# Kernel tuning notes

Measured on AMD Instinct MI355X. Metric: run time of the kernel, lower is better.

Reference implementation:

```python
import jax, jax.numpy as jnp
import numpy as np

B, T = 256, 64
L, S = 1024, 512          # large / small LSTM cell sizes
NC = 239                  # num classes
EPS = 1e-5                # BatchNorm eps (inference mode, mean=0, var=1)
TAU = 1.0                 # gumbel-softmax temperature


def setup_inputs() -> dict:
    key = jax.random.key(0)
    ks = jax.random.split(key, 12)
    def N(i, shape, s=0.05):
        return jax.random.normal(ks[i], shape, dtype=jnp.float32) * s
    return {
        "x": N(0, (B, T, 2048), 1.0),
        "x_small": N(1, (B, T, 1280), 1.0),
        # proj_mlp: Linear(2048->2048) + BN(2048) [inference] + ReLU
        "W_p": N(2, (2048, 2048)), "b_p": jnp.zeros(2048),
        "g_p": jnp.ones(2048), "be_p": jnp.zeros(2048),
        # small_proj_mlp: Linear(1280->512) + BN(512) + ReLU
        "W_s": N(3, (512, 1280)), "b_s": jnp.zeros(512),
        "g_s": jnp.ones(512), "be_s": jnp.zeros(512),
        # large LSTMCell: input 2048+512 -> hidden L
        "Wih_l": N(4, (4 * L, 2048 + 512)), "Whh_l": N(5, (4 * L, L)),
        "bih_l": jnp.zeros(4 * L), "bhh_l": jnp.zeros(4 * L),
        # small LSTMCell: input 512 -> hidden S
        "Wih_s": N(6, (4 * S, 512)), "Whh_s": N(7, (4 * S, S)),
        "bih_s": jnp.zeros(4 * S), "bhh_s": jnp.zeros(4 * S),
        # gate linear: (512 + 2L) -> 2
        "W_g": N(8, (2, 512 + 2 * L)), "b_g": jnp.zeros(2),
        # classifier: L -> NC
        "W_c": N(9, (NC, L)), "b_c": jnp.zeros(NC),
    }


def _bn_relu(x, gamma, beta):
    # inference BatchNorm1d with running_mean=0, running_var=1
    return jax.nn.relu(x * (gamma / np.sqrt(1.0 + EPS)) + beta)


def _lstm_cell(xin, h, c, Wih, Whh, bih, bhh):
    gates = xin @ Wih.T + bih + h @ Whh.T + bhh
    i, f, g, o = jnp.split(gates, 4, axis=1)
    c2 = jax.nn.sigmoid(f) * c + jax.nn.sigmoid(i) * jnp.tanh(g)
    h2 = jax.nn.sigmoid(o) * jnp.tanh(c2)
    return h2, c2


def reference(x, x_small, W_p, b_p, g_p, be_p, W_s, b_s, g_s, be_s,
              Wih_l, Whh_l, bih_l, bhh_l, Wih_s, Whh_s, bih_s, bhh_s,
              W_g, b_g, W_c, b_c):
    # project all frames at once (time-parallel part of the net)
    feats = _bn_relu(jnp.einsum('bti,oi->bto', x, W_p) + b_p, g_p, be_p)        # [B,T,2048]
    sfeats = _bn_relu(jnp.einsum('bti,oi->bto', x_small, W_s) + b_s, g_s, be_s)  # [B,T,512]

    def step(carry, ft_st):
        h_l, c_l, h_s, c_s = carry
        f_t, s_t = ft_st                                   # [B,2048], [B,512]
        h_s2, c_s2 = _lstm_cell(s_t, h_s, c_s, Wih_s, Whh_s, bih_s, bhh_s)
        # gating on OLD large state
        p = jax.nn.log_softmax(jnp.concatenate([s_t, h_l, c_l], 1) @ W_g.T + b_g, axis=1)
        y_soft = jax.nn.softmax(p / TAU, axis=1)
        y_hard = jax.nn.one_hot(jnp.argmax(y_soft, axis=1), 2, dtype=y_soft.dtype)
        r = y_hard + y_soft - jax.lax.stop_gradient(y_soft)  # straight-through hard sample
        h_ln, c_ln = _lstm_cell(jnp.concatenate([f_t, s_t], 1), h_l, c_l,
                                Wih_l, Whh_l, bih_l, bhh_l)
        ph = jnp.concatenate([h_s2[:, :S], h_l[:, S:L]], 1)  # partial (skip) hidden
        pc = jnp.concatenate([c_s2[:, :S], c_l[:, S:L]], 1)
        h_l2 = r[:, 0:1] * h_ln + r[:, 1:2] * ph
        c_l2 = r[:, 0:1] * c_ln + r[:, 1:2] * pc
        return (h_l2, c_l2, h_s2, c_s2), r

    z_l = jnp.zeros((B, L), jnp.float32)
    z_s = jnp.zeros((B, S), jnp.float32)
    (h_l, c_l, _, _), r_stack = jax.lax.scan(
        step, (z_l, z_l, z_s, z_s),
        (feats.transpose(1, 0, 2), sfeats.transpose(1, 0, 2)))
    logits = h_l @ W_c.T + b_c                             # [B,NC]
    return logits, r_stack                                 # r_stack: [T,B,2]
```

## Files before the change

kernel.cpp:

```cpp
#include <hip/hip_runtime.h>
#include <math.h>


typedef _Float16 f16;
typedef _Float16 f16x4 __attribute__((ext_vector_type(4)));
typedef _Float16 f16x8 __attribute__((ext_vector_type(8)));
typedef float f32x4 __attribute__((ext_vector_type(4)));

__device__ __forceinline__ float sigf(float x) { return 1.0f / (1.0f + expf(-x)); }

__device__ __forceinline__ void gload16(const f16* g, f16* l) {
  __builtin_amdgcn_global_load_lds((const __attribute__((address_space(1))) void*)g,
                                   (__attribute__((address_space(3))) void*)l, 16, 0, 0);
}

__global__ __launch_bounds__(256) void pack_img(const float* __restrict__ src,
    int C, int KT, int t0, int map, f16* __restrict__ dh, f16* __restrict__ dl,
    int slots)
{
  int gid = blockIdx.x * 256 + threadIdx.x;
  if (gid >= slots) return;
  int lane = gid & 63;
  int j = (gid >> 6) & 7;
  int pk = gid >> 9;
  int p = pk / KT, kt = pk - p * KT;
  int r = p * 128 + j * 16 + (lane & 15);
  int rg = map ? (((r & 255) << 6) + t0 + (r >> 8)) : r;
  int c = kt * 32 + (lane >> 4) * 8;
  const float* s = src + (long long)rg * C + c;
  float4 v0 = *(const float4*)s, v1 = *(const float4*)(s + 4);
  f16x8 h, l;
  h[0]=(f16)v0.x; l[0]=(f16)(v0.x-(float)h[0]);
  h[1]=(f16)v0.y; l[1]=(f16)(v0.y-(float)h[1]);
  h[2]=(f16)v0.z; l[2]=(f16)(v0.z-(float)h[2]);
  h[3]=(f16)v0.w; l[3]=(f16)(v0.w-(float)h[3]);
  h[4]=(f16)v1.x; l[4]=(f16)(v1.x-(float)h[4]);
  h[5]=(f16)v1.y; l[5]=(f16)(v1.y-(float)h[5]);
  h[6]=(f16)v1.z; l[6]=(f16)(v1.z-(float)h[6]);
  h[7]=(f16)v1.w; l[7]=(f16)(v1.w-(float)h[7]);
  *(f16x8*)(dh + (long long)gid * 8) = h;
  *(f16x8*)(dl + (long long)gid * 8) = l;
}

template <int BN, int EPI>
__device__ __forceinline__ void gcore(
    int pA, int pB,
    const f16* __restrict__ Ah0, const f16* __restrict__ Al0, int KT0,
    const f16* __restrict__ Ah1, const f16* __restrict__ Al1, int KT1,
    const f16* __restrict__ Bh, const f16* __restrict__ Bl, int KTB,
    float* __restrict__ C, int ldc, const float* __restrict__ G,
    f16* __restrict__ Ch, f16* __restrict__ Cl, int KTout,
    const float* __restrict__ e0, const float* __restrict__ e1,
    const float* __restrict__ e2)
{
  constexpr int WAVES = BN / 32;
  constexpr int WN = BN / 64;
  constexpr int NBU = BN / 16;
  constexpr int U = 16 + BN / 8;
  constexpr int NU = U / WAVES;
  __shared__ __align__(16) f16 smem[2][U * 512];

  const int tid = threadIdx.x;
  const int w = tid >> 6, lane = tid & 63;
  const int wr = w / WN, wc = w % WN;
  const int fr = lane & 15, fq = lane >> 4;
  const int nt = KT0 + KT1;

  const f16* up[NU];
  auto setptrs = [&](int kt) {
#pragma unroll
    for (int i = 0; i < NU; ++i) {
      const int u = w * NU + i;
      const f16* src;
      if (u < 16) {
        const int j = u & 7;
        const f16* AH = Ah0; const f16* AL = Al0; int KT = KT0, ktl = kt;
        if (KT1 > 0 && kt >= KT0) { AH = Ah1; AL = Al1; KT = KT1; ktl = kt - KT0; }
        src = ((u < 8) ? AH : AL) + (((long long)pA * KT + ktl) * 8 + j) * 512;
      } else {
        const int j = u - 16;
        const f16* IMG = (j < NBU) ? Bh : Bl;
        const int jb = (j < NBU) ? j : j - NBU;
        const int panel = pB * (BN / 128) + (jb >> 3);
        src = IMG + (((long long)panel * KTB + kt) * 8 + (jb & 7)) * 512;
      }
      up[i] = src + lane * 8;
    }
  };
  auto stage = [&](int buf) {
#pragma unroll
    for (int i = 0; i < NU; ++i) {
      gload16(up[i], &smem[buf][(w * NU + i) * 512]);
      up[i] += 4096;
    }
  };

  f32x4 acc[4][4];
#pragma unroll
  for (int m = 0; m < 4; ++m)
#pragma unroll
    for (int n = 0; n < 4; ++n) acc[m][n] = (f32x4){0.f, 0.f, 0.f, 0.f};

  setptrs(0);
  stage(0);
  __syncthreads();
  int cur = 0;
  for (int kt = 0; kt < nt; ++kt) {
    if (kt + 1 < nt) {
      if (KT1 > 0 && kt + 1 == KT0) setptrs(kt + 1);
      stage(cur ^ 1);
    }
    const f16* sb = smem[cur];
    f16x8 bh_[4], bl_[4];
#pragma unroll
    for (int n = 0; n < 4; ++n) {
      const int jb = wc * 4 + n;
      bh_[n] = *(const f16x8*)&sb[(16 + jb) * 512 + lane * 8];
      bl_[n] = *(const f16x8*)&sb[(16 + NBU + jb) * 512 + lane * 8];
    }
#pragma unroll
    for (int m = 0; m < 4; ++m) {
      const int ja = wr * 4 + m;
      f16x8 ah = *(const f16x8*)&sb[ja * 512 + lane * 8];
      f16x8 al = *(const f16x8*)&sb[(8 + ja) * 512 + lane * 8];
#pragma unroll
      for (int n = 0; n < 4; ++n) {
        acc[m][n] = __builtin_amdgcn_mfma_f32_16x16x32_f16(ah, bh_[n], acc[m][n], 0, 0, 0);
        acc[m][n] = __builtin_amdgcn_mfma_f32_16x16x32_f16(ah, bl_[n], acc[m][n], 0, 0, 0);
        acc[m][n] = __builtin_amdgcn_mfma_f32_16x16x32_f16(al, bh_[n], acc[m][n], 0, 0, 0);
      }
    }
    __syncthreads();
    cur ^= 1;
  }

  if constexpr (EPI == 1 || EPI == 2) {
#pragma unroll
    for (int m = 0; m < 4; ++m) {
#pragma unroll
      for (int n = 0; n < 4; ++n) {
        const int col = pB * BN + wc * 64 + n * 16 + fr;
        const float add = (EPI == 1) ? (e0[col] + e1[col]) : 0.f;
#pragma unroll
        for (int r = 0; r < 4; ++r) {
          const int row = pA * 128 + wr * 64 + m * 16 + fq * 4 + r;
          const long long idx = (long long)row * ldc + col;
          float v = acc[m][n][r] + add;
          if (EPI == 2) v += G[idx];
          C[idx] = v;
        }
      }
    }
  } else {
    float* cb = (float*)smem;
    const int CBLD = 132;
    for (int h = 0; h < 2; ++h) {
      if (wr == h) {
#pragma unroll
        for (int m = 0; m < 4; ++m) {
#pragma unroll
          for (int n = 0; n < 4; ++n) {
            const int colL = wc * 64 + n * 16 + fr;
            const int colG = pB * 128 + colL;
            const float p0 = e0[colG], p1 = e1[colG] * 0.99999500003750f,
                        p2 = e2[colG];
#pragma unroll
            for (int r = 0; r < 4; ++r) {
              const int rq = m * 16 + fq * 4 + r;
              cb[rq * CBLD + colL] = fmaxf((acc[m][n][r] + p0) * p1 + p2, 0.f);
            }
          }
        }
      }
      __syncthreads();
#pragma unroll
      for (int jl = 0; jl < 4; ++jl) {
        const float* s = &cb[(jl * 16 + fr) * CBLD + w * 32 + fq * 8];
        float4 v0 = *(const float4*)s, v1 = *(const float4*)(s + 4);
        float vv[8] = {v0.x, v0.y, v0.z, v0.w, v1.x, v1.y, v1.z, v1.w};
        f16x8 hh, ll;
#pragma unroll
        for (int e = 0; e < 8; ++e) {
          hh[e] = (f16)vv[e]; ll[e] = (f16)(vv[e] - (float)hh[e]);
        }
        const long long o =
            (((long long)pA * KTout + pB * 4 + w) * 8 + (h * 4 + jl)) * 512
            + lane * 8;
        *(f16x8*)(Ch + o) = hh;
        *(f16x8*)(Cl + o) = ll;
      }
      __syncthreads();
    }
  }
}

template <int BN, int EPI>
__global__ __launch_bounds__(BN * 2) void gmm_k(
    int gB, int swz,
    const f16* __restrict__ Ah0, const f16* __restrict__ Al0, int KT0,
    const f16* __restrict__ Ah1, const f16* __restrict__ Al1, int KT1,
    const f16* __restrict__ Bh, const f16* __restrict__ Bl, int KTB,
    float* __restrict__ C, int ldc, const float* __restrict__ G,
    f16* __restrict__ Ch, f16* __restrict__ Cl, int KTout,
    const float* __restrict__ e0, const float* __restrict__ e1,
    const float* __restrict__ e2)
{
  const int lin = blockIdx.x;
  int pA, pB;
  if (swz) {
    const int xc = lin & 7, j = lin >> 3, cpx = gB >> 3;
    pB = xc * cpx + (j % cpx);
    pA = j / cpx;
  } else {
    pB = lin % gB;
    pA = lin / gB;
  }
  gcore<BN, EPI>(pA, pB, Ah0, Al0, KT0, Ah1, Al1, KT1, Bh, Bl, KTB,
                 C, ldc, G, Ch, Cl, KTout, e0, e1, e2);
}

__global__ __launch_bounds__(256) void stepg_k(
    const f16* __restrict__ hlh, const f16* __restrict__ hll,
    const f16* __restrict__ hsh, const f16* __restrict__ hsl,
    const f16* __restrict__ Whlh, const f16* __restrict__ Whll,
    const f16* __restrict__ Whsh, const f16* __restrict__ Whsl,
    const float* __restrict__ Gl, const float* __restrict__ Gs,
    float* __restrict__ gl, float* __restrict__ gs)
{
  const int lin = blockIdx.x;
  const int xc = lin & 7, j = lin >> 3;
  const f16 *Ah, *Al, *Bh, *Bl;
  const float* G; float* C;
  int KT, ldc, pA, pB;
  if (j < 8) {
    pA = j >> 2; pB = xc * 4 + (j & 3);
    Ah = hlh; Al = hll; Bh = Whlh; Bl = Whll; KT = 32; ldc = 4096;
    C = gl; G = Gl;
  } else {
    const int jj = j - 8;
    pA = jj >> 1; pB = xc * 2 + (jj & 1);
    Ah = hsh; Al = hsl; Bh = Whsh; Bl = Whsl; KT = 16; ldc = 2048;
    C = gs; G = Gs;
  }
  gcore<128, 2>(pA, pB, Ah, Al, KT, nullptr, nullptr, 0, Bh, Bl, KT,
                C, ldc, G, nullptr, nullptr, 0, nullptr, nullptr, nullptr);
}

__global__ __launch_bounds__(256) void zs_img_k(const f16* __restrict__ sfh,
    const f16* __restrict__ sfl, const float* __restrict__ Wg,
    float* __restrict__ zs, int t0)
{
  const int wv = threadIdx.x >> 6, lane = threadIdx.x & 63;
  const int rr = blockIdx.x * 4 + wv;
  const int p = rr >> 7, j = (rr >> 4) & 7, fr = rr & 15;
  const int kt = lane >> 2, fq = lane & 3;
  const long long a = (((long long)p * 16 + kt) * 8 + j) * 512 + (fq * 16 + fr) * 8;
  f16x8 h8 = *(const f16x8*)(sfh + a);
  f16x8 l8 = *(const f16x8*)(sfl + a);
  const int k0 = kt * 32 + fq * 8;
  float z0 = 0.f, z1 = 0.f;
#pragma unroll
  for (int i = 0; i < 8; ++i) {
    float s = (float)h8[i] + (float)l8[i];
    z0 += s * Wg[k0 + i]; z1 += s * Wg[2560 + k0 + i];
  }
#pragma unroll
  for (int off = 32; off > 0; off >>= 1) {
    z0 += __shfl_down(z0, off);
    z1 += __shfl_down(z1, off);
  }
  if (lane == 0) {
    const int bt = ((rr & 255) << 6) + t0 + (rr >> 8);
    zs[bt * 2] = z0; zs[bt * 2 + 1] = z1;
  }
}

__global__ __launch_bounds__(256) void step_upd(
    const float* __restrict__ gl, const float* __restrict__ gs,
    const float* __restrict__ hl_o, const float* __restrict__ cl_o,
    const float* __restrict__ cs_o,
    float* __restrict__ hl_n, float* __restrict__ cl_n,
    float* __restrict__ hs_n, float* __restrict__ cs_n,
    f16* __restrict__ hlIh, f16* __restrict__ hlIl,
    f16* __restrict__ hsIh, f16* __restrict__ hsIl,
    const float* __restrict__ zs, const float* __restrict__ Wg,
    const float* __restrict__ bg, float* __restrict__ rout, int t)
{
  const int b = blockIdx.x, tid = threadIdx.x;
  __shared__ float red0[256], red1[256];
  __shared__ float shs[512], scs[512];
  __shared__ float rsh[2];

  const int pb = b >> 7, jb = (b >> 4) & 7, frb = b & 15;

  float4 h4 = *(const float4*)(hl_o + (long long)b * 1024 + tid * 4);
  float4 c4 = *(const float4*)(cl_o + (long long)b * 1024 + tid * 4);
  float4 w0h = *(const float4*)(Wg + 512 + tid * 4);
  float4 w0c = *(const float4*)(Wg + 1536 + tid * 4);
  float4 w1h = *(const float4*)(Wg + 2560 + 512 + tid * 4);
  float4 w1c = *(const float4*)(Wg + 2560 + 1536 + tid * 4);
  red0[tid] = h4.x * w0h.x + h4.y * w0h.y + h4.z * w0h.z + h4.w * w0h.w
            + c4.x * w0c.x + c4.y * w0c.y + c4.z * w0c.z + c4.w * w0c.w;
  red1[tid] = h4.x * w1h.x + h4.y * w1h.y + h4.z * w1h.z + h4.w * w1h.w
            + c4.x * w1c.x + c4.y * w1c.y + c4.z * w1c.z + c4.w * w1c.w;

  {
    const float* gb = gs + (long long)b * 2048;
#pragma unroll
    for (int e = 0; e < 2; ++e) {
      const int n = tid * 2 + e;
      float gi = gb[n], gf = gb[512 + n], gg = gb[1024 + n], go = gb[1536 + n];
      float c2 = sigf(gf) * cs_o[b * 512 + n] + sigf(gi) * tanhf(gg);
      float h2 = sigf(go) * tanhf(c2);
      shs[n] = h2; scs[n] = c2;
      hs_n[b * 512 + n] = h2; cs_n[b * 512 + n] = c2;
      const int kt = n >> 5, fqn = (n >> 3) & 3, en = n & 7;
      const long long o = (((long long)pb * 16 + kt) * 8 + jb) * 512
                        + (fqn * 16 + frb) * 8 + en;
      f16 hh = (f16)h2;
      hsIh[o] = hh; hsIl[o] = (f16)(h2 - (float)hh);
    }
  }
  __syncthreads();
  for (int s = 128; s > 0; s >>= 1) {
    if (tid < s) { red0[tid] += red0[tid + s]; red1[tid] += red1[tid + s]; }
    __syncthreads();
  }
  if (tid == 0) {
    float z0 = red0[0] + zs[(b * 64 + t) * 2 + 0] + bg[0];
    float z1 = red1[0] + zs[(b * 64 + t) * 2 + 1] + bg[1];
    int hard = (z1 > z0) ? 1 : 0;
    rsh[0] = hard ? 0.0f : 1.0f; rsh[1] = hard ? 1.0f : 0.0f;
    rout[b * 2 + 0] = rsh[0]; rout[b * 2 + 1] = rsh[1];
  }
  __syncthreads();
  const float r0 = rsh[0], r1 = rsh[1];

  {
    const float* glb = gl + (long long)b * 4096;
    const int n = tid * 4;
    float4 gi4 = *(const float4*)(glb + n);
    float4 gf4 = *(const float4*)(glb + 1024 + n);
    float4 gg4 = *(const float4*)(glb + 2048 + n);
    float4 go4 = *(const float4*)(glb + 3072 + n);
    float4 co4 = *(const float4*)(cl_o + (long long)b * 1024 + n);
    float4 ho4 = *(const float4*)(hl_o + (long long)b * 1024 + n);
    float gi[4] = {gi4.x, gi4.y, gi4.z, gi4.w};
    float gf[4] = {gf4.x, gf4.y, gf4.z, gf4.w};
    float gg[4] = {gg4.x, gg4.y, gg4.z, gg4.w};
    float go[4] = {go4.x, go4.y, go4.z, go4.w};
    float co[4] = {co4.x, co4.y, co4.z, co4.w};
    float ho[4] = {ho4.x, ho4.y, ho4.z, ho4.w};
    float hv[4], cv[4];
    f16x4 ih, il;
#pragma unroll
    for (int e = 0; e < 4; ++e) {
      float cln = sigf(gf[e]) * co[e] + sigf(gi[e]) * tanhf(gg[e]);
      float hln = sigf(go[e]) * tanhf(cln);
      float ph = (n + e < 512) ? shs[n + e] : ho[e];
      float pc = (n + e < 512) ? scs[n + e] : co[e];
      hv[e] = r0 * hln + r1 * ph;
      cv[e] = r0 * cln + r1 * pc;
      ih[e] = (f16)hv[e]; il[e] = (f16)(hv[e] - (float)ih[e]);
    }
    float4 hw = {hv[0], hv[1], hv[2], hv[3]};
    float4 cw = {cv[0], cv[1], cv[2], cv[3]};
    *(float4*)(hl_n + (long long)b * 1024 + n) = hw;
    *(float4*)(cl_n + (long long)b * 1024 + n) = cw;
    const int kt = n >> 5, fqn = (n >> 3) & 3, en = n & 7;
    const long long o = (((long long)pb * 32 + kt) * 8 + jb) * 512
                      + (fqn * 16 + frb) * 8 + en;
    *(f16x4*)(hlIh + o) = ih;
    *(f16x4*)(hlIl + o) = il;
  }
}

__global__ __launch_bounds__(256) void logits_k(const float* __restrict__ hl,
                                                const float* __restrict__ Wc,
                                                const float* __restrict__ bc,
                                                float* __restrict__ out)
{
  __shared__ float hsd[1024];
  const int b = blockIdx.x, tid = threadIdx.x;
  *(float4*)(hsd + tid * 4) = *(const float4*)(hl + (long long)b * 1024 + tid * 4);
  __syncthreads();
  if (tid < 239) {
    const float* w = Wc + (long long)tid * 1024;
    float s = 0.0f;
    for (int k = 0; k < 1024; k += 4) {
      float4 wv = *(const float4*)(w + k);
      s += hsd[k] * wv.x + hsd[k + 1] * wv.y + hsd[k + 2] * wv.z + hsd[k + 3] * wv.w;
    }
    out[(long long)b * 239 + tid] = s + bc[tid];
  }
}

#define BKK 32
template <int BM, int BN, int TM, int TN, int EPI>
__global__ __launch_bounds__(256) void gemm_nt(
    int M, int N,
    const float* __restrict__ A0, long long as0, const float* __restrict__ B0, long long bs0, int K0,
    const float* __restrict__ A1, long long as1, const float* __restrict__ B1, long long bs1, int K1,
    const float* __restrict__ A2, long long as2, const float* __restrict__ B2, long long bs2, int K2,
    float* __restrict__ C, long long ldc,
    const float* __restrict__ e0, const float* __restrict__ e1, const float* __restrict__ e2)
{
  __shared__ float As[BKK][BM + 4];
  __shared__ float Bs[BKK][BN + 4];
  const int tid = threadIdx.x;
  const int m0 = blockIdx.x * BM;
  const int n0 = blockIdx.y * BN;
  constexpr int C4 = BKK / 4;
  constexpr int RPP = 256 / C4;
  constexpr int APASS = BM / RPP;
  constexpr int BPASS = BN / RPP;
  const int lr = tid / C4;
  const int lc = tid % C4;
  float4 pa[APASS], pb[BPASS];
  const int nt = (K0 + K1 + K2) / BKK;
  auto load = [&](int kt) {
    const int kg = kt * BKK;
    const float* ap; long long as_; const float* bp; long long bs_;
    if (kg < K0)           { ap = A0 + kg;          as_ = as0; bp = B0 + kg;          bs_ = bs0; }
    else if (kg < K0 + K1) { int kl = kg - K0;      ap = A1 + kl; as_ = as1; bp = B1 + kl; bs_ = bs1; }
    else                   { int kl = kg - K0 - K1; ap = A2 + kl; as_ = as2; bp = B2 + kl; bs_ = bs2; }
#pragma unroll
    for (int p = 0; p < APASS; p++) {
      int r = lr + p * RPP;
      pa[p] = *(const float4*)(ap + (long long)(m0 + r) * as_ + lc * 4);
    }
#pragma unroll
    for (int p = 0; p < BPASS; p++) {
      int r = lr + p * RPP;
      pb[p] = *(const float4*)(bp + (long long)(n0 + r) * bs_ + lc * 4);
    }
  };
  const int tx = tid % (BN / TN);
  const int ty = tid / (BN / TN);
  float acc[TM][TN];
#pragma unroll
  for (int i = 0; i < TM; i++)
#pragma unroll
    for (int j = 0; j < TN; j++) acc[i][j] = 0.0f;
  load(0);
  for (int kt = 0; kt < nt; ++kt) {
    __syncthreads();
#pragma unroll
    for (int p = 0; p < APASS; p++) {
      int r = lr + p * RPP;
      As[lc * 4 + 0][r] = pa[p].x; As[lc * 4 + 1][r] = pa[p].y;
      As[lc * 4 + 2][r] = pa[p].z; As[lc * 4 + 3][r] = pa[p].w;
    }
#pragma unroll
    for (int p = 0; p < BPASS; p++) {
      int r = lr + p * RPP;
      Bs[lc * 4 + 0][r] = pb[p].x; Bs[lc * 4 + 1][r] = pb[p].y;
      Bs[lc * 4 + 2][r] = pb[p].z; Bs[lc * 4 + 3][r] = pb[p].w;
    }
    __syncthreads();
    if (kt + 1 < nt) load(kt + 1);
#pragma unroll
    for (int k = 0; k < BKK; k++) {
      float a[TM], bfr[TN];
#pragma unroll
      for (int i = 0; i < TM; i++) a[i] = As[k][ty * TM + i];
#pragma unroll
      for (int j = 0; j < TN; j++) bfr[j] = Bs[k][tx * TN + j];
#pragma unroll
      for (int i = 0; i < TM; i++)
#pragma unroll
        for (int j = 0; j < TN; j++) acc[i][j] += a[i] * bfr[j];
    }
  }
#pragma unroll
  for (int i = 0; i < TM; i++) {
    const int m = m0 + ty * TM + i;
    const int n = n0 + tx * TN;
    float v[TN];
#pragma unroll
    for (int j = 0; j < TN; j++) {
      float a = acc[i][j];
      if (EPI == 0) {
        float s = e1[n + j] * 0.999995f;
        a = (a + e0[n + j]) * s + e2[n + j];
        a = fmaxf(a, 0.0f);
      } else {
        a = a + e0[n + j] + e1[n + j];
      }
      v[j] = a;
    }
    float4 o; o.x = v[0]; o.y = v[1]; o.z = v[2]; o.w = v[3];
    *(float4*)(C + (long long)m * ldc + n) = o;
  }
}

__global__ __launch_bounds__(256) void zs32_k(const float* __restrict__ sf,
                                              const float* __restrict__ Wg,
                                              float* __restrict__ zs)
{
  const int wave = threadIdx.x >> 6, lane = threadIdx.x & 63;
  const int row = blockIdx.x * 4 + wave;
  const float* s = sf + (long long)row * 512 + lane * 8;
  const float* w0 = Wg + lane * 8;
  const float* w1 = Wg + 2560 + lane * 8;
  float4 sa = *(const float4*)s, sb = *(const float4*)(s + 4);
  float4 a0 = *(const float4*)w0, b0 = *(const float4*)(w0 + 4);
  float4 a1 = *(const float4*)w1, b1 = *(const float4*)(w1 + 4);
  float z0 = sa.x * a0.x + sa.y * a0.y + sa.z * a0.z + sa.w * a0.w
           + sb.x * b0.x + sb.y * b0.y + sb.z * b0.z + sb.w * b0.w;
  float z1 = sa.x * a1.x + sa.y * a1.y + sa.z * a1.z + sa.w * a1.w
           + sb.x * b1.x + sb.y * b1.y + sb.z * b1.z + sb.w * b1.w;
#pragma unroll
  for (int off = 32; off > 0; off >>= 1) {
    z0 += __shfl_down(z0, off);
    z1 += __shfl_down(z1, off);
  }
  if (lane == 0) { zs[row * 2] = z0; zs[row * 2 + 1] = z1; }
}

__global__ __launch_bounds__(256) void step_upd32(
    const float* __restrict__ gl, const float* __restrict__ gs,
    const float* __restrict__ hl_o, const float* __restrict__ cl_o,
    const float* __restrict__ cs_o,
    float* __restrict__ hl_n, float* __restrict__ cl_n,
    float* __restrict__ hs_n, float* __restrict__ cs_n,
    const float* __restrict__ zs, const float* __restrict__ Wg,
    const float* __restrict__ bg, float* __restrict__ rout, int t)
{
  const int b = blockIdx.x, tid = threadIdx.x;
  __shared__ float red0[256], red1[256];
  __shared__ float shs[512], scs[512];
  __shared__ float rsh[2];
  float4 h4 = *(const float4*)(hl_o + (long long)b * 1024 + tid * 4);
  float4 c4 = *(const float4*)(cl_o + (long long)b * 1024 + tid * 4);
  float4 w0h = *(const float4*)(Wg + 512 + tid * 4);
  float4 w0c = *(const float4*)(Wg + 1536 + tid * 4);
  float4 w1h = *(const float4*)(Wg + 2560 + 512 + tid * 4);
  float4 w1c = *(const float4*)(Wg + 2560 + 1536 + tid * 4);
  red0[tid] = h4.x * w0h.x + h4.y * w0h.y + h4.z * w0h.z + h4.w * w0h.w
            + c4.x * w0c.x + c4.y * w0c.y + c4.z * w0c.z + c4.w * w0c.w;
  red1[tid] = h4.x * w1h.x + h4.y * w1h.y + h4.z * w1h.z + h4.w * w1h.w
            + c4.x * w1c.x + c4.y * w1c.y + c4.z * w1c.z + c4.w * w1c.w;
  {
    const float* gb = gs + (long long)b * 2048;
#pragma unroll
    for (int e = 0; e < 2; ++e) {
      const int n = tid * 2 + e;
      float gi = gb[n], gf = gb[512 + n], gg = gb[1024 + n], go = gb[1536 + n];
      float c2 = sigf(gf) * cs_o[b * 512 + n] + sigf(gi) * tanhf(gg);
      float h2 = sigf(go) * tanhf(c2);
      shs[n] = h2; scs[n] = c2;
      hs_n[b * 512 + n] = h2; cs_n[b * 512 + n] = c2;
    }
  }
  __syncthreads();
  for (int s = 128; s > 0; s >>= 1) {
    if (tid < s) { red0[tid] += red0[tid + s]; red1[tid] += red1[tid + s]; }
    __syncthreads();
  }
  if (tid == 0) {
    float z0 = red0[0] + zs[(b * 64 + t) * 2 + 0] + bg[0];
    float z1 = red1[0] + zs[(b * 64 + t) * 2 + 1] + bg[1];
    int hard = (z1 > z0) ? 1 : 0;
    rsh[0] = hard ? 0.0f : 1.0f; rsh[1] = hard ? 1.0f : 0.0f;
    rout[b * 2 + 0] = rsh[0]; rout[b * 2 + 1] = rsh[1];
  }
  __syncthreads();
  const float r0 = rsh[0], r1 = rsh[1];
  {
    const float* glb = gl + (long long)b * 4096;
    const int n = tid * 4;
    float4 gi4 = *(const float4*)(glb + n);
    float4 gf4 = *(const float4*)(glb + 1024 + n);
    float4 gg4 = *(const float4*)(glb + 2048 + n);
    float4 go4 = *(const float4*)(glb + 3072 + n);
    float4 co4 = *(const float4*)(cl_o + (long long)b * 1024 + n);
    float4 ho4 = *(const float4*)(hl_o + (long long)b * 1024 + n);
    float gi[4] = {gi4.x, gi4.y, gi4.z, gi4.w};
    float gf[4] = {gf4.x, gf4.y, gf4.z, gf4.w};
    float gg[4] = {gg4.x, gg4.y, gg4.z, gg4.w};
    float go[4] = {go4.x, go4.y, go4.z, go4.w};
    float co[4] = {co4.x, co4.y, co4.z, co4.w};
    float ho[4] = {ho4.x, ho4.y, ho4.z, ho4.w};
    float hv[4], cv[4];
#pragma unroll
    for (int e = 0; e < 4; ++e) {
      float cln = sigf(gf[e]) * co[e] + sigf(gi[e]) * tanhf(gg[e]);
      float hln = sigf(go[e]) * tanhf(cln);
      float ph = (n + e < 512) ? shs[n + e] : ho[e];
      float pc = (n + e < 512) ? scs[n + e] : co[e];
      hv[e] = r0 * hln + r1 * ph;
      cv[e] = r0 * cln + r1 * pc;
    }
    float4 hw = {hv[0], hv[1], hv[2], hv[3]};
    float4 cw = {cv[0], cv[1], cv[2], cv[3]};
    *(float4*)(hl_n + (long long)b * 1024 + n) = hw;
    *(float4*)(cl_n + (long long)b * 1024 + n) = cw;
  }
}

extern "C" void kernel_launch(void* const* d_in, const int* in_sizes, int n_in,
                              void* d_out, int out_size, void* d_ws, size_t ws_size,
                              hipStream_t stream)
{
  const float* x     = (const float*)d_in[0];
  const float* xs    = (const float*)d_in[1];
  const float* W_p   = (const float*)d_in[2];
  const float* b_p   = (const float*)d_in[3];
  const float* g_p   = (const float*)d_in[4];
  const float* be_p  = (const float*)d_in[5];
  const float* W_s   = (const float*)d_in[6];
  const float* b_s   = (const float*)d_in[7];
  const float* g_s   = (const float*)d_in[8];
  const float* be_s  = (const float*)d_in[9];
  const float* Wih_l = (const float*)d_in[10];
  const float* Whh_l = (const float*)d_in[11];
  const float* bih_l = (const float*)d_in[12];
  const float* bhh_l = (const float*)d_in[13];
  const float* Wih_s = (const float*)d_in[14];
  const float* Whh_s = (const float*)d_in[15];
  const float* bih_s = (const float*)d_in[16];
  const float* bhh_s = (const float*)d_in[17];
  const float* W_g   = (const float*)d_in[18];
  const float* b_g   = (const float*)d_in[19];
  const float* W_c   = (const float*)d_in[20];
  const float* b_c   = (const float*)d_in[21];
  float* out = (float*)d_out;
  float* r_out = out + 61184;

  const int BT = 16384;
  const size_t FIXEDB = 100794368ULL;
  const size_t CHUNKB = 12320768ULL;
  int Tp = 0;
  for (int T = 64; T >= 1; T >>= 1)
    if (FIXEDB + CHUNKB * (size_t)T + 65536 <= ws_size) { Tp = T; break; }

  if (Tp > 0) {
    char* base = (char*)d_ws;
    size_t off = 0;
    auto alloc = [&](size_t n) { void* p = base + off; off += (n + 255) & ~255ULL; return p; };
    f16* WpI[2]  = {(f16*)alloc(8388608),  (f16*)alloc(8388608)};
    f16* WsI[2]  = {(f16*)alloc(1310720),  (f16*)alloc(1310720)};
    f16* WilI[2] = {(f16*)alloc(20971520), (f16*)alloc(20971520)};
    f16* WisI[2] = {(f16*)alloc(2097152),  (f16*)alloc(2097152)};
    f16* WhlI[2] = {(f16*)alloc(8388608),  (f16*)alloc(8388608)};
    f16* WhsI[2] = {(f16*)alloc(2097152),  (f16*)alloc(2097152)};
    f16* hlI[2] = {(f16*)alloc(524288), (f16*)alloc(524288)};
    f16* hsI[2] = {(f16*)alloc(262144), (f16*)alloc(262144)};
    float* zs  = (float*)alloc(131072);
    float* hl[2] = {(float*)alloc(1048576), (float*)alloc(1048576)};
    float* cl[2] = {(float*)alloc(1048576), (float*)alloc(1048576)};
    float* hsb[2] = {(float*)alloc(524288), (float*)alloc(524288)};
    float* csb[2] = {(float*)alloc(524288), (float*)alloc(524288)};
    float* gates_l = (float*)alloc(4194304);
    float* gates_s = (float*)alloc(2097152);
    f16* xI[2]  = {(f16*)alloc(1048576ULL * Tp), (f16*)alloc(1048576ULL * Tp)};
    f16* xsI[2] = {(f16*)alloc(655360ULL * Tp),  (f16*)alloc(655360ULL * Tp)};
    f16* feI[2] = {(f16*)alloc(1048576ULL * Tp), (f16*)alloc(1048576ULL * Tp)};
    f16* sfI[2] = {(f16*)alloc(262144ULL * Tp),  (f16*)alloc(262144ULL * Tp)};
    float* GxlC = (float*)alloc(4194304ULL * Tp);
    float* GxsC = (float*)alloc(2097152ULL * Tp);

    pack_img<<<2048, 256, 0, stream>>>(W_p,   2048, 64, 0, 0, WpI[0],  WpI[1],  524288);
    pack_img<<<320,  256, 0, stream>>>(W_s,   1280, 40, 0, 0, WsI[0],  WsI[1],  81920);
    pack_img<<<5120, 256, 0, stream>>>(Wih_l, 2560, 80, 0, 0, WilI[0], WilI[1], 1310720);
    pack_img<<<512,  256, 0, stream>>>(Wih_s, 512,  16, 0, 0, WisI[0], WisI[1], 131072);
    pack_img<<<2048, 256, 0, stream>>>(Whh_l, 1024, 32, 0, 0, WhlI[0], WhlI[1], 524288);
    pack_img<<<512,  256, 0, stream>>>(Whh_s, 512,  16, 0, 0, WhsI[0], WhsI[1], 131072);

    hipMemsetAsync(hl[0], 0, 1048576, stream);
    hipMemsetAsync(cl[0], 0, 1048576, stream);
    hipMemsetAsync(hsb[0], 0, 524288, stream);
    hipMemsetAsync(csb[0], 0, 524288, stream);
    hipMemsetAsync(hlI[0], 0, 524288, stream);
    hipMemsetAsync(hlI[1], 0, 524288, stream);
    hipMemsetAsync(hsI[0], 0, 262144, stream);
    hipMemsetAsync(hsI[1], 0, 262144, stream);

    const int rows = 256 * Tp;
    const int gA = rows / 128;
    for (int t0 = 0; t0 < 64; t0 += Tp) {
      pack_img<<<rows * 2048 / 8 / 256, 256, 0, stream>>>(
          x, 2048, 64, t0, 1, xI[0], xI[1], rows * 256);
      pack_img<<<rows * 1280 / 8 / 256, 256, 0, stream>>>(
          xs, 1280, 40, t0, 1, xsI[0], xsI[1], rows * 160);
      gmm_k<128, 0><<<gA * 4, 256, 0, stream>>>(
          4, 0,
          xsI[0], xsI[1], 40, nullptr, nullptr, 0,
          WsI[0], WsI[1], 40,
          nullptr, 0, nullptr, sfI[0], sfI[1], 16, b_s, g_s, be_s);
      zs_img_k<<<rows / 4, 256, 0, stream>>>(sfI[0], sfI[1], W_g, zs, t0);
      gmm_k<128, 0><<<gA * 16, 256, 0, stream>>>(
          16, 1,
          xI[0], xI[1], 64, nullptr, nullptr, 0,
          WpI[0], WpI[1], 64,
          nullptr, 0, nullptr, feI[0], feI[1], 64, b_p, g_p, be_p);
      gmm_k<256, 1><<<gA * 16, 512, 0, stream>>>(
          16, 1,
          feI[0], feI[1], 64, sfI[0], sfI[1], 16,
          WilI[0], WilI[1], 80,
          GxlC, 4096, nullptr, nullptr, nullptr, 0, bih_l, bhh_l, nullptr);
      gmm_k<128, 1><<<gA * 16, 256, 0, stream>>>(
          16, 1,
          sfI[0], sfI[1], 16, nullptr, nullptr, 0,
          WisI[0], WisI[1], 16,
          GxsC, 2048, nullptr, nullptr, nullptr, 0, bih_s, bhh_s, nullptr);

      for (int tt = 0; tt < Tp; ++tt) {
        const int t = t0 + tt;
        const int o = t & 1, nw = o ^ 1;
        stepg_k<<<96, 256, 0, stream>>>(
            hlI[0], hlI[1], hsI[0], hsI[1],
            WhlI[0], WhlI[1], WhsI[0], WhsI[1],
            GxlC + (long long)tt * 256 * 4096, GxsC + (long long)tt * 256 * 2048,
            gates_l, gates_s);
        step_upd<<<256, 256, 0, stream>>>(
            gates_l, gates_s, hl[o], cl[o], csb[o],
            hl[nw], cl[nw], hsb[nw], csb[nw],
            hlI[0], hlI[1], hsI[0], hsI[1],
            zs, W_g, b_g, r_out + (long long)t * 512, t);
      }
    }
    logits_k<<<256, 256, 0, stream>>>(hl[0], W_c, b_c, out);
    return;
  }

  float* ws = (float*)d_ws;
  size_t offf = 0;
  auto allocf = [&](size_t n) { float* p = ws + offf; offf += n; return p; };
  float* feats   = allocf((size_t)BT * 2048);
  float* sfeats  = allocf((size_t)BT * 512);
  float* zs      = allocf((size_t)BT * 2);
  float* gates_l = allocf((size_t)256 * 4096);
  float* gates_s = allocf((size_t)256 * 2048);
  float* hl[2] = { allocf(256 * 1024), allocf(256 * 1024) };
  float* cl[2] = { allocf(256 * 1024), allocf(256 * 1024) };
  float* hsb[2] = { allocf(256 * 512),  allocf(256 * 512) };
  float* csb[2] = { allocf(256 * 512),  allocf(256 * 512) };

  hipMemsetAsync(hl[0], 0, 256 * 1024 * sizeof(float), stream);
  hipMemsetAsync(cl[0], 0, 256 * 1024 * sizeof(float), stream);
  hipMemsetAsync(hsb[0], 0, 256 * 512 * sizeof(float), stream);
  hipMemsetAsync(csb[0], 0, 256 * 512 * sizeof(float), stream);

  gemm_nt<128, 64, 8, 4, 0><<<dim3(BT / 128, 2048 / 64), 256, 0, stream>>>(
      BT, 2048, x, 2048, W_p, 2048, 2048,
      nullptr, 0, nullptr, 0, 0, nullptr, 0, nullptr, 0, 0,
      feats, 2048, b_p, g_p, be_p);
  gemm_nt<128, 64, 8, 4, 0><<<dim3(BT / 128, 512 / 64), 256, 0, stream>>>(
      BT, 512, xs, 1280, W_s, 1280, 1280,
      nullptr, 0, nullptr, 0, 0, nullptr, 0, nullptr, 0, 0,
      sfeats, 512, b_s, g_s, be_s);
  zs32_k<<<BT / 4, 256, 0, stream>>>(sfeats, W_g, zs);

  for (int t = 0; t < 64; ++t) {
    const int o = t & 1, nw = o ^ 1;
    gemm_nt<64, 64, 4, 4, 1><<<dim3(4, 2048 / 64), 256, 0, stream>>>(
        256, 2048, sfeats + (long long)t * 512, 64LL * 512, Wih_s, 512, 512,
        hsb[o], 512, Whh_s, 512, 512, nullptr, 0, nullptr, 0, 0,
        gates_s, 2048, bih_s, bhh_s, nullptr);
    gemm_nt<64, 64, 4, 4, 1><<<dim3(4, 4096 / 64), 256, 0, stream>>>(
        256, 4096, feats + (long long)t * 2048, 64LL * 2048, Wih_l, 2560, 2048,
        sfeats + (long long)t * 512, 64LL * 512, Wih_l + 2048, 2560, 512,
        hl[o], 1024, Whh_l, 1024, 1024,
        gates_l, 4096, bih_l, bhh_l, nullptr);
    step_upd32<<<256, 256, 0, stream>>>(
        gates_l, gates_s, hl[o], cl[o], csb[o],
        hl[nw], cl[nw], hsb[nw], csb[nw],
        zs, W_g, b_g, r_out + (long long)t * 512, t);
  }
  logits_k<<<256, 256, 0, stream>>>(hl[0], W_c, b_c, out);
}
```

Baseline: 4.094 ms.

## Triple-buffer GEMM LDS staging with vmcnt waits and 2D XCD tile swizzle

The batched projection GEMM core moves from double to triple buffering of the LDS staging area. It prefetches two k-tiles ahead and uses explicit s_waitcnt vmcnt counts plus raw barriers instead of full __syncthreads, so global-to-LDS loads overlap more MFMA work. The block-to-tile swizzle now splits both the A and B tile dimensions across the 8 XCDs (4x2) to improve L2 reuse, and it is enabled for the small projection GEMM too. This raises LDS usage per block, which may lower occupancy. The hardcoded vmcnt values depend on NU and assume gA is even.

```diff
diff --git a/kernel.cpp b/kernel.cpp
--- a/kernel.cpp
+++ b/kernel.cpp
@@ -6,6 +6,8 @@
 typedef _Float16 f16x4 __attribute__((ext_vector_type(4)));
 typedef _Float16 f16x8 __attribute__((ext_vector_type(8)));
 typedef float f32x4 __attribute__((ext_vector_type(4)));
+
+#define WAITV(n) asm volatile("s_waitcnt vmcnt(" #n ")" ::: "memory")
 
 __device__ __forceinline__ float sigf(float x) { return 1.0f / (1.0f + expf(-x)); }
 
@@ -58,7 +60,7 @@
   constexpr int NBU = BN / 16;
   constexpr int U = 16 + BN / 8;
   constexpr int NU = U / WAVES;
-  __shared__ __align__(16) f16 smem[2][U * 512];
+  __shared__ __align__(16) f16 smem[3][U * 512];
 
   const int tid = threadIdx.x;
   const int w = tid >> 6, lane = tid & 63;
@@ -103,14 +105,26 @@
 
   setptrs(0);
   stage(0);
-  __syncthreads();
-  int cur = 0;
+  if (nt > 1) {
+    if (KT1 > 0 && KT0 == 1) setptrs(1);
+    stage(1);
+  }
+
   for (int kt = 0; kt < nt; ++kt) {
-    if (kt + 1 < nt) {
-      if (KT1 > 0 && kt + 1 == KT0) setptrs(kt + 1);
-      stage(cur ^ 1);
-    }
-    const f16* sb = smem[cur];
+    if (kt + 2 < nt) {
+      if (KT1 > 0 && kt + 2 == KT0) setptrs(kt + 2);
+      stage((kt + 2) % 3);
+    }
+    if (kt + 2 < nt) {
+      if constexpr (NU == 6) WAITV(12); else WAITV(16);
+    } else if (kt + 1 < nt) {
+      if constexpr (NU == 6) WAITV(6); else WAITV(8);
+    } else {
+      WAITV(0);
+    }
+    __builtin_amdgcn_s_barrier();
+    __builtin_amdgcn_sched_barrier(0);
+    const f16* sb = smem[kt % 3];
     f16x8 bh_[4], bl_[4];
 #pragma unroll
     for (int n = 0; n < 4; ++n) {
@@ -130,8 +144,7 @@
         acc[m][n] = __builtin_amdgcn_mfma_f32_16x16x32_f16(al, bh_[n], acc[m][n], 0, 0, 0);
       }
     }
-    __syncthreads();
-    cur ^= 1;
+    __builtin_amdgcn_s_barrier();
   }
 
   if constexpr (EPI == 1 || EPI == 2) {
@@ -196,7 +209,7 @@
 
 template <int BN, int EPI>
 __global__ __launch_bounds__(BN * 2) void gmm_k(
-    int gB, int swz,
+    int gA, int gB, int swz,
     const f16* __restrict__ Ah0, const f16* __restrict__ Al0, int KT0,
     const f16* __restrict__ Ah1, const f16* __restrict__ Al1, int KT1,
     const f16* __restrict__ Bh, const f16* __restrict__ Bl, int KTB,
@@ -208,9 +221,11 @@
   const int lin = blockIdx.x;
   int pA, pB;
   if (swz) {
-    const int xc = lin & 7, j = lin >> 3, cpx = gB >> 3;
-    pB = xc * cpx + (j % cpx);
-    pA = j / cpx;
+    const int xcd = lin & 7;
+    const int j = lin >> 3;
+    const int pbp = gB >> 2;
+    pB = (xcd & 3) * pbp + (j % pbp);
+    pA = (xcd >> 2) * (gA >> 1) + (j / pbp);
   } else {
     pB = lin % gB;
     pA = lin / gB;
@@ -685,23 +700,23 @@
       pack_img<<<rows * 1280 / 8 / 256, 256, 0, stream>>>(
           xs, 1280, 40, t0, 1, xsI[0], xsI[1], rows * 160);
       gmm_k<128, 0><<<gA * 4, 256, 0, stream>>>(
-          4, 0,
+          gA, 4, 1,
           xsI[0], xsI[1], 40, nullptr, nullptr, 0,
           WsI[0], WsI[1], 40,
           nullptr, 0, nullptr, sfI[0], sfI[1], 16, b_s, g_s, be_s);
       zs_img_k<<<rows / 4, 256, 0, stream>>>(sfI[0], sfI[1], W_g, zs, t0);
       gmm_k<128, 0><<<gA * 16, 256, 0, stream>>>(
-          16, 1,
+          gA, 16, 1,
           xI[0], xI[1], 64, nullptr, nullptr, 0,
           WpI[0], WpI[1], 64,
           nullptr, 0, nullptr, feI[0], feI[1], 64, b_p, g_p, be_p);
       gmm_k<256, 1><<<gA * 16, 512, 0, stream>>>(
-          16, 1,
+          gA, 16, 1,
           feI[0], feI[1], 64, sfI[0], sfI[1], 16,
           WilI[0], WilI[1], 80,
           GxlC, 4096, nullptr, nullptr, nullptr, 0, bih_l, bhh_l, nullptr);
       gmm_k<128, 1><<<gA * 16, 256, 0, stream>>>(
-          16, 1,
+          gA, 16, 1,
           sfI[0], sfI[1], 16, nullptr, nullptr, 0,
           WisI[0], WisI[1], 16,
           GxsC, 2048, nullptr, nullptr, nullptr, 0, bih_s, bhh_s, nullptr);
```

After: 4.324 ms. 5.6% more time.

## Use 256x256 tiles for the large input-gate GEMM and remap blocks across XCDs

Applied to the files above, without the earlier changes.

Adds a dedicated gmm256 kernel that computes 256x256 output tiles with 8 waves and 128 KB of LDS double buffering, replacing the 128x256 tile for the large LSTM input projection. Each staged A and B panel is reused across more MFMAs, which cuts global/L2 traffic per FLOP. A new cohort_map spreads blocks over the 8 XCDs in 2x4 cohorts of A and B panels to improve L2 locality, and is now also applied to the small projection GEMM. The trade-offs are one block per CU, high register pressure from 32 accumulators per thread, and fewer blocks in the grid.

```diff
diff --git a/kernel.cpp b/kernel.cpp
--- a/kernel.cpp
+++ b/kernel.cpp
@@ -12,6 +12,20 @@
 __device__ __forceinline__ void gload16(const f16* g, f16* l) {
   __builtin_amdgcn_global_load_lds((const __attribute__((address_space(1))) void*)g,
                                    (__attribute__((address_space(3))) void*)l, 16, 0, 0);
+}
+
+__device__ __forceinline__ void cohort_map(int lin, int gA, int gB, int swz,
+                                           int& pA, int& pB) {
+  if (swz && (gA & 1) == 0 && (gB & 3) == 0) {
+    const int xcd = lin & 7;
+    const int j = lin >> 3;
+    const int pbp = gB >> 2;
+    pB = (xcd & 3) * pbp + (j % pbp);
+    pA = (xcd >> 2) * (gA >> 1) + (j / pbp);
+  } else {
+    pB = lin % gB;
+    pA = lin / gB;
+  }
 }
 
 __global__ __launch_bounds__(256) void pack_img(const float* __restrict__ src,
@@ -42,7 +56,90 @@
   *(f16x8*)(dl + (long long)gid * 8) = l;
 }
 
-template <int BN, int EPI>
+template <int EPI>
+__global__ __launch_bounds__(512, 1) void gmm256(
+    int gA, int gB, int swz,
+    const f16* __restrict__ Ah0, const f16* __restrict__ Al0, int KT0,
+    const f16* __restrict__ Ah1, const f16* __restrict__ Al1, int KT1,
+    const f16* __restrict__ Bh, const f16* __restrict__ Bl, int KTB,
+    float* __restrict__ C, int ldc,
+    const float* __restrict__ e0, const float* __restrict__ e1)
+{
+  __shared__ __align__(16) char smem[131072];
+  f16 (*sm)[4][8192] = (f16 (*)[4][8192])smem;
+  const int tid = threadIdx.x;
+  const int w = tid >> 6, lane = tid & 63;
+  const int wr = w >> 2, wc = w & 3;
+  const int fr = lane & 15, fq = lane >> 4;
+  int pA, pB;
+  cohort_map(blockIdx.x, gA, gB, swz, pA, pB);
+  const int sarr = w >> 1, shalf = w & 1;
+
+  const int nt = KT0 + KT1;
+
+  auto stage = [&](int buf, int kt) {
+    const f16* base;
+    if (sarr >= 2) {
+      base = ((sarr == 2) ? Bh : Bl) + ((long long)(pB * 2 + shalf) * KTB + kt) * 4096;
+    } else if (kt < KT0) {
+      base = ((sarr == 0) ? Ah0 : Al0) + ((long long)(pA * 2 + shalf) * KT0 + kt) * 4096;
+    } else {
+      base = ((sarr == 0) ? Ah1 : Al1) + ((long long)(pA * 2 + shalf) * KT1 + (kt - KT0)) * 4096;
+    }
+    f16* dst = &sm[buf][sarr][shalf * 4096];
+#pragma unroll
+    for (int j = 0; j < 8; ++j)
+      gload16(base + j * 512 + lane * 8, dst + j * 512);
+  };
+
+  f32x4 acc[8][4];
+#pragma unroll
+  for (int m = 0; m < 8; ++m)
+#pragma unroll
+    for (int n = 0; n < 4; ++n) acc[m][n] = (f32x4){0.f, 0.f, 0.f, 0.f};
+
+  stage(0, 0);
+  __syncthreads();
+  int cur = 0;
+  for (int kt = 0; kt < nt; ++kt) {
+    if (kt + 1 < nt) stage(cur ^ 1, kt + 1);
+    f16x8 bh_[4], bl_[4];
+#pragma unroll
+    for (int n = 0; n < 4; ++n) {
+      bh_[n] = *(const f16x8*)&sm[cur][2][(wc * 4 + n) * 512 + lane * 8];
+      bl_[n] = *(const f16x8*)&sm[cur][3][(wc * 4 + n) * 512 + lane * 8];
+    }
+#pragma unroll
+    for (int m = 0; m < 8; ++m) {
+      f16x8 ah = *(const f16x8*)&sm[cur][0][wr * 4096 + m * 512 + lane * 8];
+      f16x8 al = *(const f16x8*)&sm[cur][1][wr * 4096 + m * 512 + lane * 8];
+#pragma unroll
+      for (int n = 0; n < 4; ++n) {
+        acc[m][n] = __builtin_amdgcn_mfma_f32_16x16x32_f16(ah, bh_[n], acc[m][n], 0, 0, 0);
+        acc[m][n] = __builtin_amdgcn_mfma_f32_16x16x32_f16(ah, bl_[n], acc[m][n], 0, 0, 0);
+        acc[m][n] = __builtin_amdgcn_mfma_f32_16x16x32_f16(al, bh_[n], acc[m][n], 0, 0, 0);
+      }
+    }
+    __syncthreads();
+    cur ^= 1;
+  }
+
+#pragma unroll
+  for (int m = 0; m < 8; ++m) {
+#pragma unroll
+    for (int n = 0; n < 4; ++n) {
+      const int col = pB * 256 + wc * 64 + n * 16 + fr;
+      const float add = e0[col] + e1[col];
+#pragma unroll
+      for (int r = 0; r < 4; ++r) {
+        const int row = pA * 256 + wr * 128 + m * 16 + fq * 4 + r;
+        C[(long long)row * ldc + col] = acc[m][n][r] + add;
+      }
+    }
+  }
+}
+
+template <int EPI>
 __device__ __forceinline__ void gcore(
     int pA, int pB,
     const f16* __restrict__ Ah0, const f16* __restrict__ Al0, int KT0,
@@ -53,16 +150,13 @@
     const float* __restrict__ e0, const float* __restrict__ e1,
     const float* __restrict__ e2)
 {
-  constexpr int WAVES = BN / 32;
-  constexpr int WN = BN / 64;
-  constexpr int NBU = BN / 16;
-  constexpr int U = 16 + BN / 8;
-  constexpr int NU = U / WAVES;
+  constexpr int U = 32;
+  constexpr int NU = 8;
   __shared__ __align__(16) f16 smem[2][U * 512];
 
   const int tid = threadIdx.x;
   const int w = tid >> 6, lane = tid & 63;
-  const int wr = w / WN, wc = w % WN;
+  const int wr = w >> 1, wc = w & 1;
   const int fr = lane & 15, fq = lane >> 4;
   const int nt = KT0 + KT1;
 
@@ -79,10 +173,9 @@
         src = ((u < 8) ? AH : AL) + (((long long)pA * KT + ktl) * 8 + j) * 512;
       } else {
         const int j = u - 16;
-        const f16* IMG = (j < NBU) ? Bh : Bl;
-        const int jb = (j < NBU) ? j : j - NBU;
-        const int panel = pB * (BN / 128) + (jb >> 3);
-        src = IMG + (((long long)panel * KTB + kt) * 8 + (jb & 7)) * 512;
+        const f16* IMG = (j < 8) ? Bh : Bl;
+        const int jb = j & 7;
+        src = IMG + (((long long)pB * KTB + kt) * 8 + jb) * 512;
       }
       up[i] = src + lane * 8;
     }
@@ -116,7 +209,7 @@
     for (int n = 0; n < 4; ++n) {
       const int jb = wc * 4 + n;
       bh_[n] = *(const f16x8*)&sb[(16 + jb) * 512 + lane * 8];
-      bl_[n] = *(const f16x8*)&sb[(16 + NBU + jb) * 512 + lane * 8];
+      bl_[n] = *(const f16x8*)&sb[(24 + jb) * 512 + lane * 8];
     }
 #pragma unroll
     for (int m = 0; m < 4; ++m) {
@@ -139,7 +232,7 @@
     for (int m = 0; m < 4; ++m) {
 #pragma unroll
       for (int n = 0; n < 4; ++n) {
-        const int col = pB * BN + wc * 64 + n * 16 + fr;
+        const int col = pB * 128 + wc * 64 + n * 16 + fr;
         const float add = (EPI == 1) ? (e0[col] + e1[col]) : 0.f;
 #pragma unroll
         for (int r = 0; r < 4; ++r) {
@@ -194,9 +287,9 @@
   }
 }
 
-template <int BN, int EPI>
-__global__ __launch_bounds__(BN * 2) void gmm_k(
-    int gB, int swz,
+template <int EPI>
+__global__ __launch_bounds__(256) void gmm_k(
+    int gA, int gB, int swz,
     const f16* __restrict__ Ah0, const f16* __restrict__ Al0, int KT0,
     const f16* __restrict__ Ah1, const f16* __restrict__ Al1, int KT1,
     const f16* __restrict__ Bh, const f16* __restrict__ Bl, int KTB,
@@ -205,18 +298,10 @@
     const float* __restrict__ e0, const float* __restrict__ e1,
     const float* __restrict__ e2)
 {
-  const int lin = blockIdx.x;
   int pA, pB;
-  if (swz) {
-    const int xc = lin & 7, j = lin >> 3, cpx = gB >> 3;
-    pB = xc * cpx + (j % cpx);
-    pA = j / cpx;
-  } else {
-    pB = lin % gB;
-    pA = lin / gB;
-  }
-  gcore<BN, EPI>(pA, pB, Ah0, Al0, KT0, Ah1, Al1, KT1, Bh, Bl, KTB,
-                 C, ldc, G, Ch, Cl, KTout, e0, e1, e2);
+  cohort_map(blockIdx.x, gA, gB, swz, pA, pB);
+  gcore<EPI>(pA, pB, Ah0, Al0, KT0, Ah1, Al1, KT1, Bh, Bl, KTB,
+             C, ldc, G, Ch, Cl, KTout, e0, e1, e2);
 }
 
 __global__ __launch_bounds__(256) void stepg_k(
@@ -242,8 +327,8 @@
     Ah = hsh; Al = hsl; Bh = Whsh; Bl = Whsl; KT = 16; ldc = 2048;
     C = gs; G = Gs;
   }
-  gcore<128, 2>(pA, pB, Ah, Al, KT, nullptr, nullptr, 0, Bh, Bl, KT,
-                C, ldc, G, nullptr, nullptr, 0, nullptr, nullptr, nullptr);
+  gcore<2>(pA, pB, Ah, Al, KT, nullptr, nullptr, 0, Bh, Bl, KT,
+           C, ldc, G, nullptr, nullptr, 0, nullptr, nullptr, nullptr);
 }
 
 __global__ __launch_bounds__(256) void zs_img_k(const f16* __restrict__ sfh,
@@ -678,30 +763,31 @@
     hipMemsetAsync(hsI[1], 0, 262144, stream);
 
     const int rows = 256 * Tp;
-    const int gA = rows / 128;
+    const int gA1 = rows / 128;
+    const int gA2 = rows / 256;
     for (int t0 = 0; t0 < 64; t0 += Tp) {
       pack_img<<<rows * 2048 / 8 / 256, 256, 0, stream>>>(
           x, 2048, 64, t0, 1, xI[0], xI[1], rows * 256);
       pack_img<<<rows * 1280 / 8 / 256, 256, 0, stream>>>(
           xs, 1280, 40, t0, 1, xsI[0], xsI[1], rows * 160);
-      gmm_k<128, 0><<<gA * 4, 256, 0, stream>>>(
-          4, 0,
+      gmm_k<0><<<gA1 * 4, 256, 0, stream>>>(
+          gA1, 4, 1,
           xsI[0], xsI[1], 40, nullptr, nullptr, 0,
           WsI[0], WsI[1], 40,
           nullptr, 0, nullptr, sfI[0], sfI[1], 16, b_s, g_s, be_s);
       zs_img_k<<<rows / 4, 256, 0, stream>>>(sfI[0], sfI[1], W_g, zs, t0);
-      gmm_k<128, 0><<<gA * 16, 256, 0, stream>>>(
-          16, 1,
+      gmm_k<0><<<gA1 * 16, 256, 0, stream>>>(
+          gA1, 16, 1,
           xI[0], xI[1], 64, nullptr, nullptr, 0,
           WpI[0], WpI[1], 64,
           nullptr, 0, nullptr, feI[0], feI[1], 64, b_p, g_p, be_p);
-      gmm_k<256, 1><<<gA * 16, 512, 0, stream>>>(
-          16, 1,
+      gmm256<1><<<gA2 * 16, 512, 0, stream>>>(
+          gA2, 16, 1,
           feI[0], feI[1], 64, sfI[0], sfI[1], 16,
           WilI[0], WilI[1], 80,
-          GxlC, 4096, nullptr, nullptr, nullptr, 0, bih_l, bhh_l, nullptr);
-      gmm_k<128, 1><<<gA * 16, 256, 0, stream>>>(
-          16, 1,
+          GxlC, 4096, bih_l, bhh_l);
+      gmm_k<1><<<gA1 * 16, 256, 0, stream>>>(
+          gA1, 16, 1,
           sfI[0], sfI[1], 16, nullptr, nullptr, 0,
           WisI[0], WisI[1], 16,
           GxsC, 2048, nullptr, nullptr, nullptr, 0, bih_s, bhh_s, nullptr);
```

Result: no change. 4.043 ms (-1.2%).
